# Kernel tuning notes

Hardware: AMD Instinct MI355X
Metric: run time of the kernel (lower is better)

The kernel has to match this reference:

```python
import jax, jax.numpy as jnp
import numpy as np

N_QUBITS = 4
Q_DEPTH = 6
Q_DELTA = 0.01
INPUT_SIZE = 64
BATCH = 262144


def _ry_gate(theta):
    # RY(theta) = [[cos(t/2), -sin(t/2)], [sin(t/2), cos(t/2)]]; theta scalar or (B,)
    c = jnp.cos(theta / 2)
    s = jnp.sin(theta / 2)
    return jnp.stack([jnp.stack([c, -s], -1), jnp.stack([s, c], -1)], -2)


def _apply_1q(state, gate, wire):
    # state: (B,2,2,2,2); gate: (2,2) shared or (B,2,2) per-sample
    ax = wire + 1
    s = jnp.moveaxis(state, ax, -1)
    if gate.ndim == 2:
        s = jnp.einsum('ij,b...j->b...i', gate, s)
    else:
        s = jnp.einsum('bij,b...j->b...i', gate, s)
    return jnp.moveaxis(s, -1, ax)


def _apply_cnot(state, ctrl, tgt):
    ca, ta = ctrl + 1, tgt + 1
    s0 = jnp.take(state, jnp.array([0]), axis=ca)
    s1 = jnp.take(state, jnp.array([1]), axis=ca)
    s1 = jnp.flip(s1, axis=ta)  # X on target where control=1
    return jnp.concatenate([s0, s1], axis=ca)


def _quantum_net(q_in, q_weights):
    # q_in: (B, 4) per-sample RY angles; q_weights: (Q_DEPTH, 4)
    B = q_in.shape[0]
    # H layer on |0000>: uniform real amplitude 1/4 over all 16 basis states
    state = jnp.full((B,) + (2,) * N_QUBITS, 0.25, dtype=q_in.dtype)
    for w in range(N_QUBITS):
        state = _apply_1q(state, _ry_gate(q_in[:, w]), w)
    for k in range(Q_DEPTH):
        for i in range(0, N_QUBITS - 1, 2):
            state = _apply_cnot(state, i, i + 1)
        for i in range(1, N_QUBITS - 1, 2):
            state = _apply_cnot(state, i, i + 1)
        for w in range(N_QUBITS):
            state = _apply_1q(state, _ry_gate(q_weights[k, w]), w)
    # All gates are real -> real statevector; probs = amp^2
    probs = state * state
    signs = jnp.array([1.0, -1.0], dtype=state.dtype)
    expz = []
    for w in range(N_QUBITS):
        shp = [1] * (N_QUBITS + 1)
        shp[w + 1] = 2
        expz.append(jnp.sum(probs * signs.reshape(shp), axis=tuple(range(1, N_QUBITS + 1))))
    return jnp.stack(expz, axis=-1)  # (B, 4)


def setup_inputs() -> dict:
    key = jax.random.key(0)
    k1, k2, k3, k4, k5, k6 = jax.random.split(key, 6)
    bound_pre = 1.0 / np.sqrt(INPUT_SIZE)
    bound_post = 1.0 / np.sqrt(N_QUBITS)
    return {
        'input_features': jax.random.normal(k1, (BATCH, INPUT_SIZE), dtype=jnp.float32),
        'pre_w': jax.random.uniform(k2, (N_QUBITS, INPUT_SIZE), jnp.float32, -bound_pre, bound_pre),
        'pre_b': jax.random.uniform(k3, (N_QUBITS,), jnp.float32, -bound_pre, bound_pre),
        'q_params': Q_DELTA * jax.random.normal(k4, (Q_DEPTH * N_QUBITS,), dtype=jnp.float32),
        'post_w': jax.random.uniform(k5, (1, N_QUBITS), jnp.float32, -bound_post, bound_post),
        'post_b': jax.random.uniform(k6, (1,), jnp.float32, -bound_post, bound_post),
    }


def reference(input_features, pre_w, pre_b, q_params, post_w, post_b):
    pre_out = input_features @ pre_w.T + pre_b
    q_in = jnp.tanh(pre_out) * (jnp.pi / 2.0)
    q_out = _quantum_net(q_in, q_params.reshape(Q_DEPTH, N_QUBITS))
    return q_out @ post_w.T + post_b  # (B, 1)
```

## Files before the change

kernel.cpp:

```cpp
#include <hip/hip_runtime.h>
#include <math.h>

#define NQ      4
#define QDEPTH  6
#define TPB     256
#define ROWLEN  64

__device__ __forceinline__ float fast_tanh(float x) {
    float e = __expf(2.0f * x);
    float r = __builtin_amdgcn_rcpf(e + 1.0f);
    return fmaf(-2.0f, r, 1.0f);
}

__device__ __forceinline__ void lds_fence_barrier() {
    asm volatile("s_waitcnt lgkmcnt(0)" ::: "memory");
    __builtin_amdgcn_s_barrier();
}

template<int W>
__device__ __forceinline__ void apply_ry(float st[16], float c, float s) {
    constexpr int M = 8 >> W;
#pragma unroll
    for (int i = 0; i < 16; ++i) {
        if ((i & M) == 0) {
            float a0 = st[i];
            float a1 = st[i | M];
            st[i]     = fmaf(c, a0, -(s * a1));
            st[i | M] = fmaf(s, a0,  (c * a1));
        }
    }
}

template<int C, int T>
__device__ __forceinline__ void apply_cnot(float st[16]) {
    constexpr int MC = 8 >> C;
    constexpr int MT = 8 >> T;
#pragma unroll
    for (int i = 0; i < 16; ++i) {
        if ((i & MC) != 0 && (i & MT) == 0) {
            float tmp = st[i];
            st[i] = st[i | MT];
            st[i | MT] = tmp;
        }
    }
}

__global__ __launch_bounds__(TPB, 4) void dqnet_kernel(
    const float* __restrict__ inp,
    const float* __restrict__ pre_w,
    const float* __restrict__ pre_b,
    const float* __restrict__ qp,
    const float* __restrict__ post_w,
    const float* __restrict__ post_b,
    float* __restrict__ out)
{
    __shared__ float4 tile[4 * 512];
    __shared__ float cs[QDEPTH * NQ], sn[QDEPTH * NQ], gg[16];
    __shared__ float Ush[16][16];
    __shared__ float Msh[16][16];
    __shared__ float S1[192], S2[144], S3[108];
    __shared__ float Tsh[81];

    const int t = threadIdx.x;
    const int wave = t >> 6;
    const int lane = t & 63;
    const size_t wrow0 = (size_t)blockIdx.x * TPB + wave * 64;
    const float4* gp = (const float4*)(inp + wrow0 * ROWLEN);
    float4* wt = &tile[wave * 512];
    const float4* pw4 = (const float4*)pre_w;

    float4 x0[8], x1[8];
#pragma unroll
    for (int j = 0; j < 8; ++j) {
        int idx = j * 64 + lane;
        int rw = idx >> 3, c = idx & 7;
        x0[j] = gp[rw * 16 + c];
    }
#pragma unroll
    for (int j = 0; j < 8; ++j) {
        int idx = j * 64 + lane;
        int rw = idx >> 3, c = idx & 7;
        x1[j] = gp[rw * 16 + 8 + c];
    }

    if (t < QDEPTH * NQ) {
        float h = 0.5f * qp[t];
        cs[t] = __cosf(h);
        sn[t] = __sinf(h);
    } else if (t >= 32 && t < 48) {
        int i = t - 32;
        float v = 0.0f;
#pragma unroll
        for (int w = 0; w < NQ; ++w) {
            float p = post_w[w];
            v += ((i >> (3 - w)) & 1) ? -p : p;
        }
        gg[i] = v;
    }
    lds_fence_barrier();

    if (t < 16) {
        float st[16];
#pragma unroll
        for (int i = 0; i < 16; ++i) st[i] = (i == t) ? 1.0f : 0.0f;
#pragma unroll
        for (int k = 0; k < QDEPTH; ++k) {
            apply_cnot<0, 1>(st);
            apply_cnot<2, 3>(st);
            apply_cnot<1, 2>(st);
            apply_ry<0>(st, cs[k * 4 + 0], sn[k * 4 + 0]);
            apply_ry<1>(st, cs[k * 4 + 1], sn[k * 4 + 1]);
            apply_ry<2>(st, cs[k * 4 + 2], sn[k * 4 + 2]);
            apply_ry<3>(st, cs[k * 4 + 3], sn[k * 4 + 3]);
        }
#pragma unroll
        for (int k = 0; k < 16; ++k) Ush[k][t] = st[k];
    }
    lds_fence_barrier();

    {
        int i = t >> 4, j = t & 15;
        float m = 0.0f;
#pragma unroll
        for (int k = 0; k < 16; ++k)
            m = fmaf(gg[k] * Ush[k][i], Ush[k][j], m);
        Msh[i][j] = m;
    }
    lds_fence_barrier();

    if (t < 192) {
        int e0 = t >> 6, r = t & 63;
        int p1 = r >> 4, p2 = (r >> 2) & 3, p3 = r & 3;
        auto Rv = [&](int p0) {
            int i = ((p0 >> 1) << 3) | ((p1 >> 1) << 2) | ((p2 >> 1) << 1) | (p3 >> 1);
            int j = ((p0 & 1) << 3) | ((p1 & 1) << 2) | ((p2 & 1) << 1) | (p3 & 1);
            return Msh[i][j];
        };
        float v = (e0 == 0) ? 0.5f * (Rv(0) + Rv(3))
                : (e0 == 1) ? 0.5f * (Rv(3) - Rv(0))
                            : 0.5f * (Rv(1) + Rv(2));
        S1[e0 * 64 + r] = v;
    }
    lds_fence_barrier();

    if (t < 144) {
        int e0 = t / 48, rem = t % 48;
        int e1 = rem >> 4, r2 = rem & 15;
        const float* base = &S1[e0 * 64];
        auto g1 = [&](int p1) { return base[p1 * 16 + r2]; };
        float v = (e1 == 0) ? 0.5f * (g1(0) + g1(3))
                : (e1 == 1) ? 0.5f * (g1(3) - g1(0))
                            : 0.5f * (g1(1) + g1(2));
        S2[(e0 * 3 + e1) * 16 + r2] = v;
    }
    lds_fence_barrier();

    if (t < 108) {
        int e01 = t / 12, rem = t % 12;
        int e2 = rem >> 2, p3 = rem & 3;
        const float* base = &S2[e01 * 16];
        auto g2 = [&](int p2) { return base[p2 * 4 + p3]; };
        float v = (e2 == 0) ? 0.5f * (g2(0) + g2(3))
                : (e2 == 1) ? 0.5f * (g2(3) - g2(0))
                            : 0.5f * (g2(1) + g2(2));
        S3[(e01 * 3 + e2) * 4 + p3] = v;
    }
    lds_fence_barrier();

    if (t < 81) {
        int e012 = t / 3, e3 = t % 3;
        const float* base = &S3[e012 * 4];
        float v = (e3 == 0) ? 0.5f * (base[0] + base[3])
                : (e3 == 1) ? 0.5f * (base[3] - base[0])
                            : 0.5f * (base[1] + base[2]);
        if (t == 0) v += post_b[0];
        Tsh[t] = v;
    }
    lds_fence_barrier();

#pragma unroll
    for (int j = 0; j < 8; ++j) {
        int idx = j * 64 + lane;
        int rw = idx >> 3, c = idx & 7;
        wt[rw * 8 + (c ^ (rw & 7))] = x0[j];
    }

    float acc0 = pre_b[0], acc1 = pre_b[1], acc2 = pre_b[2], acc3 = pre_b[3];
#pragma unroll
    for (int i = 0; i < 8; ++i) {
        float4 x  = wt[lane * 8 + (i ^ (lane & 7))];
        float4 w0 = pw4[0 * 16 + i];
        float4 w1 = pw4[1 * 16 + i];
        float4 w2 = pw4[2 * 16 + i];
        float4 w3 = pw4[3 * 16 + i];
        acc0 = fmaf(x.x, w0.x, acc0); acc0 = fmaf(x.y, w0.y, acc0);
        acc0 = fmaf(x.z, w0.z, acc0); acc0 = fmaf(x.w, w0.w, acc0);
        acc1 = fmaf(x.x, w1.x, acc1); acc1 = fmaf(x.y, w1.y, acc1);
        acc1 = fmaf(x.z, w1.z, acc1); acc1 = fmaf(x.w, w1.w, acc1);
        acc2 = fmaf(x.x, w2.x, acc2); acc2 = fmaf(x.y, w2.y, acc2);
        acc2 = fmaf(x.z, w2.z, acc2); acc2 = fmaf(x.w, w2.w, acc2);
        acc3 = fmaf(x.x, w3.x, acc3); acc3 = fmaf(x.y, w3.y, acc3);
        acc3 = fmaf(x.z, w3.z, acc3); acc3 = fmaf(x.w, w3.w, acc3);
    }

#pragma unroll
    for (int j = 0; j < 8; ++j) {
        int idx = j * 64 + lane;
        int rw = idx >> 3, c = idx & 7;
        wt[rw * 8 + (c ^ (rw & 7))] = x1[j];
    }
#pragma unroll
    for (int i = 0; i < 8; ++i) {
        float4 x  = wt[lane * 8 + (i ^ (lane & 7))];
        float4 w0 = pw4[0 * 16 + 8 + i];
        float4 w1 = pw4[1 * 16 + 8 + i];
        float4 w2 = pw4[2 * 16 + 8 + i];
        float4 w3 = pw4[3 * 16 + 8 + i];
        acc0 = fmaf(x.x, w0.x, acc0); acc0 = fmaf(x.y, w0.y, acc0);
        acc0 = fmaf(x.z, w0.z, acc0); acc0 = fmaf(x.w, w0.w, acc0);
        acc1 = fmaf(x.x, w1.x, acc1); acc1 = fmaf(x.y, w1.y, acc1);
        acc1 = fmaf(x.z, w1.z, acc1); acc1 = fmaf(x.w, w1.w, acc1);
        acc2 = fmaf(x.x, w2.x, acc2); acc2 = fmaf(x.y, w2.y, acc2);
        acc2 = fmaf(x.z, w2.z, acc2); acc2 = fmaf(x.w, w2.w, acc2);
        acc3 = fmaf(x.x, w3.x, acc3); acc3 = fmaf(x.y, w3.y, acc3);
        acc3 = fmaf(x.z, w3.z, acc3); acc3 = fmaf(x.w, w3.w, acc3);
    }

    const float QH = 1.57079632679489662f;
    float th0 = fast_tanh(acc0) * QH;
    float th1 = fast_tanh(acc1) * QH;
    float th2 = fast_tanh(acc2) * QH;
    float th3 = fast_tanh(acc3) * QH;
    float s0 = __sinf(th0), c0 = __cosf(th0);
    float s1 = __sinf(th1), c1 = __cosf(th1);
    float s2 = __sinf(th2), c2 = __cosf(th2);
    float s3 = __sinf(th3), c3 = __cosf(th3);

    float r = 0.0f;
#pragma unroll
    for (int e0 = 0; e0 < 3; ++e0) {
        float a0 = 0.0f;
#pragma unroll
        for (int e1 = 0; e1 < 3; ++e1) {
            float a1 = 0.0f;
#pragma unroll
            for (int e2 = 0; e2 < 3; ++e2) {
                const float* tb = &Tsh[((e0 * 3 + e1) * 3 + e2) * 3];
                float w = fmaf(c3, tb[2], fmaf(s3, tb[1], tb[0]));
                a1 = (e2 == 0) ? (a1 + w) : (e2 == 1) ? fmaf(s2, w, a1) : fmaf(c2, w, a1);
            }
            a0 = (e1 == 0) ? (a0 + a1) : (e1 == 1) ? fmaf(s1, a1, a0) : fmaf(c1, a1, a0);
        }
        r = (e0 == 0) ? (r + a0) : (e0 == 1) ? fmaf(s0, a0, r) : fmaf(c0, a0, r);
    }

    out[wrow0 + lane] = r;
}

extern "C" void kernel_launch(void* const* d_in, const int* in_sizes, int n_in,
                              void* d_out, int out_size, void* d_ws, size_t ws_size,
                              hipStream_t stream) {
    const float* inp    = (const float*)d_in[0];
    const float* pre_w  = (const float*)d_in[1];
    const float* pre_b  = (const float*)d_in[2];
    const float* qp     = (const float*)d_in[3];
    const float* post_w = (const float*)d_in[4];
    const float* post_b = (const float*)d_in[5];
    float* out = (float*)d_out;

    int n = in_sizes[0] / ROWLEN;
    int grid = n / TPB;
    dqnet_kernel<<<grid, TPB, 0, stream>>>(inp, pre_w, pre_b, qp, post_w, post_b, out);
}
```

Baseline: 126.1 us.

## Warp-specialize: dedicated fifth wave builds circuit table while four waves stream inputs

```diff
diff --git a/kernel.cpp b/kernel.cpp
--- a/kernel.cpp
+++ b/kernel.cpp
@@ -3,7 +3,7 @@
 
 #define NQ      4
 #define QDEPTH  6
-#define TPB     256
+#define TPB     320
 #define ROWLEN  64
 
 __device__ __forceinline__ float fast_tanh(float x) {
@@ -12,9 +12,8 @@
     return fmaf(-2.0f, r, 1.0f);
 }
 
-__device__ __forceinline__ void lds_fence_barrier() {
+__device__ __forceinline__ void wave_lds_fence() {
     asm volatile("s_waitcnt lgkmcnt(0)" ::: "memory");
-    __builtin_amdgcn_s_barrier();
 }
 
 template<int W>
@@ -45,7 +44,7 @@
     }
 }
 
-__global__ __launch_bounds__(TPB, 4) void dqnet_kernel(
+__global__ __launch_bounds__(TPB, 5) void dqnet_kernel(
     const float* __restrict__ inp,
     const float* __restrict__ pre_w,
     const float* __restrict__ pre_b,
@@ -59,202 +58,228 @@
     __shared__ float Ush[16][16];
     __shared__ float Msh[16][16];
     __shared__ float S1[192], S2[144], S3[108];
-    __shared__ float Tsh[81];
+    __shared__ float4 T4[27];
 
     const int t = threadIdx.x;
     const int wave = t >> 6;
     const int lane = t & 63;
-    const size_t wrow0 = (size_t)blockIdx.x * TPB + wave * 64;
-    const float4* gp = (const float4*)(inp + wrow0 * ROWLEN);
-    float4* wt = &tile[wave * 512];
-    const float4* pw4 = (const float4*)pre_w;
-
-    float4 x0[8], x1[8];
-#pragma unroll
-    for (int j = 0; j < 8; ++j) {
-        int idx = j * 64 + lane;
-        int rw = idx >> 3, c = idx & 7;
-        x0[j] = gp[rw * 16 + c];
-    }
-#pragma unroll
-    for (int j = 0; j < 8; ++j) {
-        int idx = j * 64 + lane;
-        int rw = idx >> 3, c = idx & 7;
-        x1[j] = gp[rw * 16 + 8 + c];
-    }
-
-    if (t < QDEPTH * NQ) {
-        float h = 0.5f * qp[t];
-        cs[t] = __cosf(h);
-        sn[t] = __sinf(h);
-    } else if (t >= 32 && t < 48) {
-        int i = t - 32;
-        float v = 0.0f;
-#pragma unroll
-        for (int w = 0; w < NQ; ++w) {
-            float p = post_w[w];
-            v += ((i >> (3 - w)) & 1) ? -p : p;
-        }
-        gg[i] = v;
-    }
-    lds_fence_barrier();
-
-    if (t < 16) {
-        float st[16];
-#pragma unroll
-        for (int i = 0; i < 16; ++i) st[i] = (i == t) ? 1.0f : 0.0f;
-#pragma unroll
-        for (int k = 0; k < QDEPTH; ++k) {
-            apply_cnot<0, 1>(st);
-            apply_cnot<2, 3>(st);
-            apply_cnot<1, 2>(st);
-            apply_ry<0>(st, cs[k * 4 + 0], sn[k * 4 + 0]);
-            apply_ry<1>(st, cs[k * 4 + 1], sn[k * 4 + 1]);
-            apply_ry<2>(st, cs[k * 4 + 2], sn[k * 4 + 2]);
-            apply_ry<3>(st, cs[k * 4 + 3], sn[k * 4 + 3]);
-        }
-#pragma unroll
-        for (int k = 0; k < 16; ++k) Ush[k][t] = st[k];
-    }
-    lds_fence_barrier();
-
-    {
-        int i = t >> 4, j = t & 15;
-        float m = 0.0f;
-#pragma unroll
-        for (int k = 0; k < 16; ++k)
-            m = fmaf(gg[k] * Ush[k][i], Ush[k][j], m);
-        Msh[i][j] = m;
-    }
-    lds_fence_barrier();
-
-    if (t < 192) {
-        int e0 = t >> 6, r = t & 63;
-        int p1 = r >> 4, p2 = (r >> 2) & 3, p3 = r & 3;
-        auto Rv = [&](int p0) {
-            int i = ((p0 >> 1) << 3) | ((p1 >> 1) << 2) | ((p2 >> 1) << 1) | (p3 >> 1);
-            int j = ((p0 & 1) << 3) | ((p1 & 1) << 2) | ((p2 & 1) << 1) | (p3 & 1);
-            return Msh[i][j];
-        };
-        float v = (e0 == 0) ? 0.5f * (Rv(0) + Rv(3))
-                : (e0 == 1) ? 0.5f * (Rv(3) - Rv(0))
-                            : 0.5f * (Rv(1) + Rv(2));
-        S1[e0 * 64 + r] = v;
-    }
-    lds_fence_barrier();
-
-    if (t < 144) {
-        int e0 = t / 48, rem = t % 48;
-        int e1 = rem >> 4, r2 = rem & 15;
-        const float* base = &S1[e0 * 64];
-        auto g1 = [&](int p1) { return base[p1 * 16 + r2]; };
-        float v = (e1 == 0) ? 0.5f * (g1(0) + g1(3))
-                : (e1 == 1) ? 0.5f * (g1(3) - g1(0))
-                            : 0.5f * (g1(1) + g1(2));
-        S2[(e0 * 3 + e1) * 16 + r2] = v;
-    }
-    lds_fence_barrier();
-
-    if (t < 108) {
-        int e01 = t / 12, rem = t % 12;
-        int e2 = rem >> 2, p3 = rem & 3;
-        const float* base = &S2[e01 * 16];
-        auto g2 = [&](int p2) { return base[p2 * 4 + p3]; };
-        float v = (e2 == 0) ? 0.5f * (g2(0) + g2(3))
-                : (e2 == 1) ? 0.5f * (g2(3) - g2(0))
-                            : 0.5f * (g2(1) + g2(2));
-        S3[(e01 * 3 + e2) * 4 + p3] = v;
-    }
-    lds_fence_barrier();
-
-    if (t < 81) {
-        int e012 = t / 3, e3 = t % 3;
-        const float* base = &S3[e012 * 4];
-        float v = (e3 == 0) ? 0.5f * (base[0] + base[3])
-                : (e3 == 1) ? 0.5f * (base[3] - base[0])
-                            : 0.5f * (base[1] + base[2]);
-        if (t == 0) v += post_b[0];
-        Tsh[t] = v;
-    }
-    lds_fence_barrier();
-
-#pragma unroll
-    for (int j = 0; j < 8; ++j) {
-        int idx = j * 64 + lane;
-        int rw = idx >> 3, c = idx & 7;
-        wt[rw * 8 + (c ^ (rw & 7))] = x0[j];
-    }
-
-    float acc0 = pre_b[0], acc1 = pre_b[1], acc2 = pre_b[2], acc3 = pre_b[3];
-#pragma unroll
-    for (int i = 0; i < 8; ++i) {
-        float4 x  = wt[lane * 8 + (i ^ (lane & 7))];
-        float4 w0 = pw4[0 * 16 + i];
-        float4 w1 = pw4[1 * 16 + i];
-        float4 w2 = pw4[2 * 16 + i];
-        float4 w3 = pw4[3 * 16 + i];
-        acc0 = fmaf(x.x, w0.x, acc0); acc0 = fmaf(x.y, w0.y, acc0);
-        acc0 = fmaf(x.z, w0.z, acc0); acc0 = fmaf(x.w, w0.w, acc0);
-        acc1 = fmaf(x.x, w1.x, acc1); acc1 = fmaf(x.y, w1.y, acc1);
-        acc1 = fmaf(x.z, w1.z, acc1); acc1 = fmaf(x.w, w1.w, acc1);
-        acc2 = fmaf(x.x, w2.x, acc2); acc2 = fmaf(x.y, w2.y, acc2);
-        acc2 = fmaf(x.z, w2.z, acc2); acc2 = fmaf(x.w, w2.w, acc2);
-        acc3 = fmaf(x.x, w3.x, acc3); acc3 = fmaf(x.y, w3.y, acc3);
-        acc3 = fmaf(x.z, w3.z, acc3); acc3 = fmaf(x.w, w3.w, acc3);
-    }
-
-#pragma unroll
-    for (int j = 0; j < 8; ++j) {
-        int idx = j * 64 + lane;
-        int rw = idx >> 3, c = idx & 7;
-        wt[rw * 8 + (c ^ (rw & 7))] = x1[j];
-    }
-#pragma unroll
-    for (int i = 0; i < 8; ++i) {
-        float4 x  = wt[lane * 8 + (i ^ (lane & 7))];
-        float4 w0 = pw4[0 * 16 + 8 + i];
-        float4 w1 = pw4[1 * 16 + 8 + i];
-        float4 w2 = pw4[2 * 16 + 8 + i];
-        float4 w3 = pw4[3 * 16 + 8 + i];
-        acc0 = fmaf(x.x, w0.x, acc0); acc0 = fmaf(x.y, w0.y, acc0);
-        acc0 = fmaf(x.z, w0.z, acc0); acc0 = fmaf(x.w, w0.w, acc0);
-        acc1 = fmaf(x.x, w1.x, acc1); acc1 = fmaf(x.y, w1.y, acc1);
-        acc1 = fmaf(x.z, w1.z, acc1); acc1 = fmaf(x.w, w1.w, acc1);
-        acc2 = fmaf(x.x, w2.x, acc2); acc2 = fmaf(x.y, w2.y, acc2);
-        acc2 = fmaf(x.z, w2.z, acc2); acc2 = fmaf(x.w, w2.w, acc2);
-        acc3 = fmaf(x.x, w3.x, acc3); acc3 = fmaf(x.y, w3.y, acc3);
-        acc3 = fmaf(x.z, w3.z, acc3); acc3 = fmaf(x.w, w3.w, acc3);
-    }
-
-    const float QH = 1.57079632679489662f;
-    float th0 = fast_tanh(acc0) * QH;
-    float th1 = fast_tanh(acc1) * QH;
-    float th2 = fast_tanh(acc2) * QH;
-    float th3 = fast_tanh(acc3) * QH;
-    float s0 = __sinf(th0), c0 = __cosf(th0);
-    float s1 = __sinf(th1), c1 = __cosf(th1);
-    float s2 = __sinf(th2), c2 = __cosf(th2);
-    float s3 = __sinf(th3), c3 = __cosf(th3);
-
-    float r = 0.0f;
-#pragma unroll
-    for (int e0 = 0; e0 < 3; ++e0) {
-        float a0 = 0.0f;
-#pragma unroll
-        for (int e1 = 0; e1 < 3; ++e1) {
-            float a1 = 0.0f;
-#pragma unroll
-            for (int e2 = 0; e2 < 3; ++e2) {
-                const float* tb = &Tsh[((e0 * 3 + e1) * 3 + e2) * 3];
-                float w = fmaf(c3, tb[2], fmaf(s3, tb[1], tb[0]));
-                a1 = (e2 == 0) ? (a1 + w) : (e2 == 1) ? fmaf(s2, w, a1) : fmaf(c2, w, a1);
-            }
-            a0 = (e1 == 0) ? (a0 + a1) : (e1 == 1) ? fmaf(s1, a1, a0) : fmaf(c1, a1, a0);
-        }
-        r = (e0 == 0) ? (r + a0) : (e0 == 1) ? fmaf(s0, a0, r) : fmaf(c0, a0, r);
-    }
-
-    out[wrow0 + lane] = r;
+    const size_t wrow0 = (size_t)blockIdx.x * 256 + wave * 64;
+
+    float s0, c0, s1, c1, s2, c2, s3, c3;
+
+    if (wave == 4) {
+        if (lane < QDEPTH * NQ) {
+            float h = 0.5f * qp[lane];
+            cs[lane] = __cosf(h);
+            sn[lane] = __sinf(h);
+        } else if (lane >= 32 && lane < 48) {
+            int i = lane - 32;
+            float v = 0.0f;
+#pragma unroll
+            for (int w = 0; w < NQ; ++w) {
+                float p = post_w[w];
+                v += ((i >> (3 - w)) & 1) ? -p : p;
+            }
+            gg[i] = v;
+        }
+        wave_lds_fence();
+
+        if (lane < 16) {
+            float st[16];
+#pragma unroll
+            for (int i = 0; i < 16; ++i) st[i] = (i == lane) ? 1.0f : 0.0f;
+#pragma unroll
+            for (int k = 0; k < QDEPTH; ++k) {
+                apply_cnot<0, 1>(st);
+                apply_cnot<2, 3>(st);
+                apply_cnot<1, 2>(st);
+                apply_ry<0>(st, cs[k * 4 + 0], sn[k * 4 + 0]);
+                apply_ry<1>(st, cs[k * 4 + 1], sn[k * 4 + 1]);
+                apply_ry<2>(st, cs[k * 4 + 2], sn[k * 4 + 2]);
+                apply_ry<3>(st, cs[k * 4 + 3], sn[k * 4 + 3]);
+            }
+#pragma unroll
+            for (int k = 0; k < 16; ++k) Ush[k][lane] = st[k];
+        }
+        wave_lds_fence();
+
+#pragma unroll
+        for (int it = 0; it < 4; ++it) {
+            int idx = it * 64 + lane;
+            int i = idx >> 4, j = idx & 15;
+            float m = 0.0f;
+#pragma unroll
+            for (int k = 0; k < 16; ++k)
+                m = fmaf(gg[k] * Ush[k][i], Ush[k][j], m);
+            Msh[i][j] = m;
+        }
+        wave_lds_fence();
+
+#pragma unroll
+        for (int it = 0; it < 3; ++it) {
+            int idx = it * 64 + lane;
+            int e0 = idx >> 6, r = idx & 63;
+            int p1 = r >> 4, p2 = (r >> 2) & 3, p3 = r & 3;
+            auto Rv = [&](int p0) {
+                int i = ((p0 >> 1) << 3) | ((p1 >> 1) << 2) | ((p2 >> 1) << 1) | (p3 >> 1);
+                int j = ((p0 & 1) << 3) | ((p1 & 1) << 2) | ((p2 & 1) << 1) | (p3 & 1);
+                return Msh[i][j];
+            };
+            float v = (e0 == 0) ? 0.5f * (Rv(0) + Rv(3))
+                    : (e0 == 1) ? 0.5f * (Rv(3) - Rv(0))
+                                : 0.5f * (Rv(1) + Rv(2));
+            S1[idx] = v;
+        }
+        wave_lds_fence();
+
+#pragma unroll
+        for (int it = 0; it < 3; ++it) {
+            int idx = it * 64 + lane;
+            if (idx < 144) {
+                int e0 = idx / 48, rem = idx % 48;
+                int e1 = rem >> 4, r2 = rem & 15;
+                const float* base = &S1[e0 * 64];
+                auto g1 = [&](int p1) { return base[p1 * 16 + r2]; };
+                float v = (e1 == 0) ? 0.5f * (g1(0) + g1(3))
+                        : (e1 == 1) ? 0.5f * (g1(3) - g1(0))
+                                    : 0.5f * (g1(1) + g1(2));
+                S2[(e0 * 3 + e1) * 16 + r2] = v;
+            }
+        }
+        wave_lds_fence();
+
+#pragma unroll
+        for (int it = 0; it < 2; ++it) {
+            int idx = it * 64 + lane;
+            if (idx < 108) {
+                int e01 = idx / 12, rem = idx % 12;
+                int e2 = rem >> 2, p3 = rem & 3;
+                const float* base = &S2[e01 * 16];
+                auto g2 = [&](int p2) { return base[p2 * 4 + p3]; };
+                float v = (e2 == 0) ? 0.5f * (g2(0) + g2(3))
+                        : (e2 == 1) ? 0.5f * (g2(3) - g2(0))
+                                    : 0.5f * (g2(1) + g2(2));
+                S3[(e01 * 3 + e2) * 4 + p3] = v;
+            }
+        }
+        wave_lds_fence();
+
+#pragma unroll
+        for (int it = 0; it < 2; ++it) {
+            int idx = it * 64 + lane;
+            if (idx < 108) {
+                int e3 = idx & 3, e012 = idx >> 2;
+                float v = 0.0f;
+                if (e3 < 3) {
+                    const float* base = &S3[e012 * 4];
+                    v = (e3 == 0) ? 0.5f * (base[0] + base[3])
+                      : (e3 == 1) ? 0.5f * (base[3] - base[0])
+                                  : 0.5f * (base[1] + base[2]);
+                    if (idx == 0) v += post_b[0];
+                }
+                ((float*)T4)[idx] = v;
+            }
+        }
+    } else {
+        const float4* gp = (const float4*)(inp + wrow0 * ROWLEN);
+        float4* wt = &tile[wave * 512];
+        const float4* pw4 = (const float4*)pre_w;
+
+        float4 x0[8];
+#pragma unroll
+        for (int j = 0; j < 8; ++j) {
+            int idx = j * 64 + lane;
+            int rw = idx >> 3, c = idx & 7;
+            x0[j] = gp[rw * 16 + c];
+        }
+#pragma unroll
+        for (int j = 0; j < 8; ++j) {
+            int idx = j * 64 + lane;
+            int rw = idx >> 3, c = idx & 7;
+            wt[rw * 8 + (c ^ (rw & 7))] = x0[j];
+        }
+        float4 x1[8];
+#pragma unroll
+        for (int j = 0; j < 8; ++j) {
+            int idx = j * 64 + lane;
+            int rw = idx >> 3, c = idx & 7;
+            x1[j] = gp[rw * 16 + 8 + c];
+        }
+
+        float acc0 = pre_b[0], acc1 = pre_b[1], acc2 = pre_b[2], acc3 = pre_b[3];
+#pragma unroll
+        for (int i = 0; i < 8; ++i) {
+            float4 x  = wt[lane * 8 + (i ^ (lane & 7))];
+            float4 w0 = pw4[0 * 16 + i];
+            float4 w1 = pw4[1 * 16 + i];
+            float4 w2 = pw4[2 * 16 + i];
+            float4 w3 = pw4[3 * 16 + i];
+            acc0 = fmaf(x.x, w0.x, acc0); acc0 = fmaf(x.y, w0.y, acc0);
+            acc0 = fmaf(x.z, w0.z, acc0); acc0 = fmaf(x.w, w0.w, acc0);
+            acc1 = fmaf(x.x, w1.x, acc1); acc1 = fmaf(x.y, w1.y, acc1);
+            acc1 = fmaf(x.z, w1.z, acc1); acc1 = fmaf(x.w, w1.w, acc1);
+            acc2 = fmaf(x.x, w2.x, acc2); acc2 = fmaf(x.y, w2.y, acc2);
+            acc2 = fmaf(x.z, w2.z, acc2); acc2 = fmaf(x.w, w2.w, acc2);
+            acc3 = fmaf(x.x, w3.x, acc3); acc3 = fmaf(x.y, w3.y, acc3);
+            acc3 = fmaf(x.z, w3.z, acc3); acc3 = fmaf(x.w, w3.w, acc3);
+        }
+
+#pragma unroll
+        for (int j = 0; j < 8; ++j) {
+            int idx = j * 64 + lane;
+            int rw = idx >> 3, c = idx & 7;
+            wt[rw * 8 + (c ^ (rw & 7))] = x1[j];
+        }
+#pragma unroll
+        for (int i = 0; i < 8; ++i) {
+            float4 x  = wt[lane * 8 + (i ^ (lane & 7))];
+            float4 w0 = pw4[0 * 16 + 8 + i];
+            float4 w1 = pw4[1 * 16 + 8 + i];
+            float4 w2 = pw4[2 * 16 + 8 + i];
+            float4 w3 = pw4[3 * 16 + 8 + i];
+            acc0 = fmaf(x.x, w0.x, acc0); acc0 = fmaf(x.y, w0.y, acc0);
+            acc0 = fmaf(x.z, w0.z, acc0); acc0 = fmaf(x.w, w0.w, acc0);
+            acc1 = fmaf(x.x, w1.x, acc1); acc1 = fmaf(x.y, w1.y, acc1);
+            acc1 = fmaf(x.z, w1.z, acc1); acc1 = fmaf(x.w, w1.w, acc1);
+            acc2 = fmaf(x.x, w2.x, acc2); acc2 = fmaf(x.y, w2.y, acc2);
+            acc2 = fmaf(x.z, w2.z, acc2); acc2 = fmaf(x.w, w2.w, acc2);
+            acc3 = fmaf(x.x, w3.x, acc3); acc3 = fmaf(x.y, w3.y, acc3);
+            acc3 = fmaf(x.z, w3.z, acc3); acc3 = fmaf(x.w, w3.w, acc3);
+        }
+
+        const float QH = 1.57079632679489662f;
+        float th0 = fast_tanh(acc0) * QH;
+        float th1 = fast_tanh(acc1) * QH;
+        float th2 = fast_tanh(acc2) * QH;
+        float th3 = fast_tanh(acc3) * QH;
+        s0 = __sinf(th0); c0 = __cosf(th0);
+        s1 = __sinf(th1); c1 = __cosf(th1);
+        s2 = __sinf(th2); c2 = __cosf(th2);
+        s3 = __sinf(th3); c3 = __cosf(th3);
+    }
+
+    __syncthreads();
+
+    if (wave < 4) {
+        float r = 0.0f;
+#pragma unroll
+        for (int e0 = 0; e0 < 3; ++e0) {
+            float a0 = 0.0f;
+#pragma unroll
+            for (int e1 = 0; e1 < 3; ++e1) {
+                float a1 = 0.0f;
+#pragma unroll
+                for (int e2 = 0; e2 < 3; ++e2) {
+                    float4 tb = T4[(e0 * 3 + e1) * 3 + e2];
+                    float w = fmaf(c3, tb.z, fmaf(s3, tb.y, tb.x));
+                    a1 = (e2 == 0) ? (a1 + w) : (e2 == 1) ? fmaf(s2, w, a1) : fmaf(c2, w, a1);
+                }
+                a0 = (e1 == 0) ? (a0 + a1) : (e1 == 1) ? fmaf(s1, a1, a0) : fmaf(c1, a1, a0);
+            }
+            r = (e0 == 0) ? (r + a0) : (e0 == 1) ? fmaf(s0, a0, r) : fmaf(c0, a0, r);
+        }
+        out[wrow0 + lane] = r;
+    }
 }
 
 extern "C" void kernel_launch(void* const* d_in, const int* in_sizes, int n_in,
@@ -269,6 +294,6 @@
     float* out = (float*)d_out;
 
     int n = in_sizes[0] / ROWLEN;
-    int grid = n / TPB;
+    int grid = n / 256;
     dqnet_kernel<<<grid, TPB, 0, stream>>>(inp, pre_w, pre_b, qp, post_w, post_b, out);
 }
```

New measurement: 102.3 us. -18.8%, faster.
